# Kernel tuning notes

Hardware: AMD Instinct MI355X
Metric: run time of the kernel (lower is better)

The kernel has to match this reference:

```python
import jax, jax.numpy as jnp
import numpy as np

HIDDEN = 1024
STATE = 16
EXPAND = 2
INNER = HIDDEN * EXPAND
BATCH, SEQ = 4, 2048


def setup_inputs() -> dict:
    key = jax.random.key(0)
    ks = jax.random.split(key, 12)
    s = 0.02
    return {
        "x": jax.random.normal(ks[0], (BATCH, SEQ, HIDDEN), jnp.float32),
        "norm_scale": jnp.ones((HIDDEN,), jnp.float32),
        "norm_bias": jnp.zeros((HIDDEN,), jnp.float32),
        "W_in": jax.random.normal(ks[1], (HIDDEN, 2 * INNER), jnp.float32) * s,
        "conv_w": jax.random.normal(ks[2], (INNER, 3), jnp.float32) * 0.3,
        "conv_b": jnp.zeros((INNER,), jnp.float32),
        "W_dt": jax.random.normal(ks[3], (INNER, INNER), jnp.float32) * s,
        "b_dt": jnp.zeros((INNER,), jnp.float32),
        "A_log": jax.random.normal(ks[4], (INNER, STATE), jnp.float32),
        "D_param": jnp.ones((INNER,), jnp.float32),
        "W_B": jax.random.normal(ks[5], (INNER, STATE), jnp.float32) * s,
        "W_C": jax.random.normal(ks[6], (INNER, STATE), jnp.float32) * s,
        "W_out": jax.random.normal(ks[7], (INNER, HIDDEN), jnp.float32) * s,
    }


def reference(x, norm_scale, norm_bias, W_in, conv_w, conv_b, W_dt, b_dt,
              A_log, D_param, W_B, W_C, W_out):
    residual = x
    # LayerNorm (eps = 1e-5, matches nn.LayerNorm default)
    mu = jnp.mean(x, axis=-1, keepdims=True)
    var = jnp.mean(jnp.square(x - mu), axis=-1, keepdims=True)
    xn = (x - mu) * jax.lax.rsqrt(var + 1e-5) * norm_scale + norm_bias

    xz = xn @ W_in                         # [B, L, 2*inner]
    xb, z = jnp.split(xz, 2, axis=-1)      # each [B, L, inner]

    # depthwise conv1d, kernel 3, padding 1 (cross-correlation as in torch)
    xp = jnp.pad(xb, ((0, 0), (1, 1), (0, 0)))
    xb = (conv_w[:, 0] * xp[:, :-2] + conv_w[:, 1] * xp[:, 1:-1]
          + conv_w[:, 2] * xp[:, 2:] + conv_b)
    xb = jax.nn.silu(xb)

    dt = jax.nn.softplus(xb @ W_dt + b_dt)  # [B, L, inner]
    A = -jnp.exp(A_log)                     # [inner, N]
    Bi = xb @ W_B                           # [B, L, N]
    Ci = xb @ W_C                           # [B, L, N]

    def step(h, inp):
        x_t, dt_t, B_t, C_t = inp           # [B,D], [B,D], [B,N], [B,N]
        A_bar = jnp.exp(dt_t[:, :, None] * A)                 # [B, D, N]
        h = A_bar * h + (dt_t * x_t)[:, :, None] * B_t[:, None, :]
        y_t = jnp.einsum('bdn,bn->bd', h, C_t)
        return h, y_t

    h0 = jnp.zeros((x.shape[0], INNER, STATE), x.dtype)
    xs = (jnp.swapaxes(xb, 0, 1), jnp.swapaxes(dt, 0, 1),
          jnp.swapaxes(Bi, 0, 1), jnp.swapaxes(Ci, 0, 1))
    _, y = jax.lax.scan(step, h0, xs)       # y: [L, B, D]
    y = jnp.swapaxes(y, 0, 1)

    y = (y + D_param * xb) * jax.nn.silu(z)
    return residual + y @ W_out
```

## Files before the change

kernel.cpp:

```cpp
#include <hip/hip_runtime.h>
#include <hip/hip_bf16.h>
#include <cstdint>
#include <cstddef>

#define B_DIM 4
#define L_DIM 2048
#define H_DIM 1024
#define D_DIM 2048
#define N_STATE 16
#define TOKENS (B_DIM * L_DIM)
#define CH 16
#define LC (L_DIM / CH)
#define NEXT 2304
#define NLIM2 2080

typedef __bf16 bf16x8 __attribute__((ext_vector_type(8)));
typedef float f32x4 __attribute__((ext_vector_type(4)));

__device__ __forceinline__ float sigmoidf_(float x) { return 1.f / (1.f + __expf(-x)); }
__device__ __forceinline__ float softplusf_(float x) {
  return fmaxf(x, 0.f) + log1pf(__expf(-fabsf(x)));
}
__device__ __forceinline__ void gl_lds16(const void* g, void* l) {
  __builtin_amdgcn_global_load_lds(
      (const __attribute__((address_space(1))) unsigned int*)g,
      (__attribute__((address_space(3))) unsigned int*)l, 16, 0, 0);
}

__global__ __launch_bounds__(256) void ln_kernel(const float* __restrict__ x,
    const float* __restrict__ gamma, const float* __restrict__ beta,
    __hip_bfloat16* __restrict__ out) {
  int row = blockIdx.x;
  int t = threadIdx.x;
  const float* px = x + (size_t)row * H_DIM;
  float4 v = *(const float4*)(px + t * 4);
  float s  = v.x + v.y + v.z + v.w;
  float ss = v.x * v.x + v.y * v.y + v.z * v.z + v.w * v.w;
  for (int off = 32; off > 0; off >>= 1) {
    s  += __shfl_down(s, off);
    ss += __shfl_down(ss, off);
  }
  __shared__ float red[8];
  __shared__ float stats[2];
  int wave = t >> 6, lane = t & 63;
  if (lane == 0) { red[wave] = s; red[4 + wave] = ss; }
  __syncthreads();
  if (t == 0) {
    float S  = red[0] + red[1] + red[2] + red[3];
    float SS = red[4] + red[5] + red[6] + red[7];
    float mu = S / H_DIM;
    float var = SS / H_DIM - mu * mu;
    stats[0] = mu;
    stats[1] = rsqrtf(var + 1e-5f);
  }
  __syncthreads();
  float mu = stats[0], rstd = stats[1];
  float4 g  = *(const float4*)(gamma + t * 4);
  float4 bt = *(const float4*)(beta + t * 4);
  __hip_bfloat16* po = out + (size_t)row * H_DIM + t * 4;
  po[0] = __float2bfloat16((v.x - mu) * rstd * g.x + bt.x);
  po[1] = __float2bfloat16((v.y - mu) * rstd * g.y + bt.y);
  po[2] = __float2bfloat16((v.z - mu) * rstd * g.z + bt.z);
  po[3] = __float2bfloat16((v.w - mu) * rstd * g.w + bt.w);
}

__global__ void transpose_bf16(const float* __restrict__ in,
                               __hip_bfloat16* __restrict__ out, int R, int C) {
  __shared__ float tile[32][33];
  int c0 = blockIdx.x * 32, r0 = blockIdx.y * 32;
  int tx = threadIdx.x, ty = threadIdx.y;
  for (int i = 0; i < 32; i += 8)
    tile[ty + i][tx] = in[(size_t)(r0 + ty + i) * C + c0 + tx];
  __syncthreads();
  for (int i = 0; i < 32; i += 8)
    out[(size_t)(c0 + ty + i) * R + r0 + tx] = __float2bfloat16(tile[tx][ty + i]);
}

__global__ __launch_bounds__(256) void wbc_transpose(const float* __restrict__ WB,
    const float* __restrict__ WC, __hip_bfloat16* __restrict__ Wext) {
  int tid = blockIdx.x * 256 + threadIdx.x;
  int c = tid & 31;
  int k0 = (tid >> 5) * 16;
  const float* W = (c < 16) ? WB : WC;
  int cc = c & 15;
  __hip_bfloat16* o = Wext + (size_t)(2048 + c) * D_DIM + k0;
  for (int kk = 0; kk < 16; ++kk)
    o[kk] = __float2bfloat16(W[(size_t)(k0 + kk) * N_STATE + cc]);
}

template <int MODE>
__global__ __launch_bounds__(512, 2) void gemm256(
    const __hip_bfloat16* __restrict__ A, const __hip_bfloat16* __restrict__ Bt,
    void* __restrict__ C0, void* __restrict__ C1, int nsplit, int nlimit,
    int K, int lda, int ldb, int ldc, int ntn,
    const float* __restrict__ bias, const float* __restrict__ resid) {
  __shared__ __hip_bfloat16 lds[65536];
  const int t = threadIdx.x;
  const int nwg = gridDim.x;
  int bid = blockIdx.x;
  int wgid = (bid & 7) * (nwg >> 3) + (bid >> 3);
  const int m0 = (wgid / ntn) * 256;
  const int n0 = (wgid % ntn) * 256;

  const int wave = t >> 6, lane = t & 63;
  const int wm = wave >> 2, wn = wave & 3;
  const int l16 = lane & 15, quad = lane >> 4;
  const int bh = wn >> 1;

  const int srow = t >> 3, cslot = t & 7;
  const int cdata = cslot ^ (srow & 7);
  const __hip_bfloat16* Ast = A + (size_t)(m0 + srow) * lda + cdata * 8;
  const __hip_bfloat16* Bst = Bt + (size_t)(n0 + srow) * ldb + cdata * 8;
  const int stoff = srow * 64 + cslot * 8;

  const int ch0 = quad ^ (l16 & 7);
  const int ch1 = ch0 ^ 4;
  const int aoff0 = wm * 8192 + l16 * 64 + ch0 * 8;
  const int aoff1 = wm * 8192 + l16 * 64 + ch1 * 8;
  const int boff0 = 16384 + bh * 8192 + ((wn & 1) * 64 + l16) * 64 + ch0 * 8;
  const int boff1 = 16384 + bh * 8192 + ((wn & 1) * 64 + l16) * 64 + ch1 * 8;

  const int NT = K >> 6;

#define STAGE_HT(dstb, mat, h, ktX) do {                                        \
    const __hip_bfloat16* g_ = ((mat) ? Bst : Ast)                              \
        + (size_t)((h) * 128) * ((mat) ? ldb : lda) + (size_t)(ktX) * 64;       \
    __hip_bfloat16* l_ = &lds[(dstb) + (mat) * 16384 + (h) * 8192 + stoff];     \
    gl_lds16(g_, l_);                                                           \
    gl_lds16(g_ + (size_t)64 * ((mat) ? ldb : lda), l_ + 4096);                 \
  } while (0)

#define RD_A(aP, i0, db_) do {                                                  \
    aP[0][0] = *(const bf16x8*)&lds[(db_) + aoff0 + (i0) * 1024];               \
    aP[0][1] = *(const bf16x8*)&lds[(db_) + aoff1 + (i0) * 1024];               \
    aP[1][0] = *(const bf16x8*)&lds[(db_) + aoff0 + ((i0) + 1) * 1024];         \
    aP[1][1] = *(const bf16x8*)&lds[(db_) + aoff1 + ((i0) + 1) * 1024];         \
  } while (0)

#define RD_B(db_) do {                                                          \
    _Pragma("unroll") for (int j = 0; j < 4; ++j) {                             \
      bB0[j] = *(const bf16x8*)&lds[(db_) + boff0 + j * 1024];                  \
      bB1[j] = *(const bf16x8*)&lds[(db_) + boff1 + j * 1024];                  \
    }                                                                           \
  } while (0)

#define MFMA_PAIR(aP, i0) do {                                                  \
    _Pragma("unroll") for (int j = 0; j < 4; ++j) {                             \
      acc[i0][j] = __builtin_amdgcn_mfma_f32_16x16x32_bf16(                     \
          aP[0][0], bB0[j], acc[i0][j], 0, 0, 0);                               \
      acc[i0][j] = __builtin_amdgcn_mfma_f32_16x16x32_bf16(                     \
          aP[0][1], bB1[j], acc[i0][j], 0, 0, 0);                               \
      acc[(i0) + 1][j] = __builtin_amdgcn_mfma_f32_16x16x32_bf16(               \
          aP[1][0], bB0[j], acc[(i0) + 1][j], 0, 0, 0);                         \
      acc[(i0) + 1][j] = __builtin_amdgcn_mfma_f32_16x16x32_bf16(               \
          aP[1][1], bB1[j], acc[(i0) + 1][j], 0, 0, 0);                         \
    }                                                                           \
  } while (0)

  f32x4 acc[8][4] = {};
  bf16x8 bB0[4], bB1[4];
  bf16x8 a01[2][2], a23[2][2], a45[2][2], a67[2][2];

  STAGE_HT(0, 1, 0, 0);
  STAGE_HT(0, 1, 1, 0);
  STAGE_HT(0, 0, 0, 0);
  STAGE_HT(0, 0, 1, 0);
  STAGE_HT(32768, 1, 0, 1);
  STAGE_HT(32768, 1, 1, 1);
  STAGE_HT(32768, 0, 0, 1);
  asm volatile("s_waitcnt vmcnt(6)" ::: "memory");
  __builtin_amdgcn_s_barrier();

  for (int kt = 0; kt < NT; ++kt) {
    const int db32 = (kt & 1) << 15;
    const int dn32 = db32 ^ 32768;
    const bool p1 = (kt + 1 < NT);
    const bool p2 = (kt + 2 < NT);
    RD_B(db32);
    RD_A(a01, 0, db32);
    if (p1) STAGE_HT(dn32, 0, 1, kt + 1);
    __builtin_amdgcn_s_barrier();
    __builtin_amdgcn_s_setprio(1);
    MFMA_PAIR(a01, 0);
    __builtin_amdgcn_s_setprio(0);
    __builtin_amdgcn_s_barrier();
    RD_A(a23, 2, db32);
    RD_A(a45, 4, db32);
    if (p2) STAGE_HT(db32, 1, 0, kt + 2);
    __builtin_amdgcn_s_barrier();
    __builtin_amdgcn_s_setprio(1);
    MFMA_PAIR(a23, 2);
    __builtin_amdgcn_s_setprio(0);
    __builtin_amdgcn_s_barrier();
    RD_A(a67, 6, db32);
    if (p2) STAGE_HT(db32, 1, 1, kt + 2);
    __builtin_amdgcn_s_barrier();
    __builtin_amdgcn_s_setprio(1);
    MFMA_PAIR(a45, 4);
    __builtin_amdgcn_s_setprio(0);
    __builtin_amdgcn_s_barrier();
    if (p2) STAGE_HT(db32, 0, 0, kt + 2);
    __builtin_amdgcn_s_barrier();
    __builtin_amdgcn_s_setprio(1);
    MFMA_PAIR(a67, 6);
    __builtin_amdgcn_s_setprio(0);
    if (p2) {
      asm volatile("s_waitcnt vmcnt(6)" ::: "memory");
    } else {
      asm volatile("s_waitcnt vmcnt(0)" ::: "memory");
    }
    __builtin_amdgcn_s_barrier();
  }

  const int row_base = m0 + wm * 128;
  const int col_base = n0 + wn * 64;
#pragma unroll
  for (int i = 0; i < 8; ++i) {
    const int row0 = row_base + i * 16 + quad * 4;
#pragma unroll
    for (int j = 0; j < 4; ++j) {
      const int col = col_base + j * 16 + l16;
      f32x4 v = acc[i][j];
      if (MODE == 0) {
#pragma unroll
        for (int r = 0; r < 4; ++r) {
          size_t idx = (size_t)(row0 + r) * ldc + col;
          ((float*)C0)[idx] = v[r] + resid[idx];
        }
      } else if (MODE == 1) {
        bool mainc = (col < nsplit);
        __hip_bfloat16* cb = mainc ? (__hip_bfloat16*)C0 : (__hip_bfloat16*)C1;
        int ccol = mainc ? col : col - nsplit;
#pragma unroll
        for (int r = 0; r < 4; ++r)
          cb[(size_t)(row0 + r) * ldc + ccol] = __float2bfloat16(v[r]);
      } else {
        if (col < nsplit) {
          float bb = bias[col];
#pragma unroll
          for (int r = 0; r < 4; ++r)
            ((__hip_bfloat16*)C0)[(size_t)(row0 + r) * ldc + col] =
                __float2bfloat16(softplusf_(v[r] + bb));
        } else if (col < nlimit) {
#pragma unroll
          for (int r = 0; r < 4; ++r)
            ((float*)C1)[(size_t)(row0 + r) * 128 + (col - nsplit)] = v[r];
        }
      }
    }
  }
#undef STAGE_HT
#undef RD_A
#undef RD_B
#undef MFMA_PAIR
}

#define BM 128
#define BN 128
#define BK 64

template <int MODE>
__global__ __launch_bounds__(256) void gemm_bf16(
    const __hip_bfloat16* __restrict__ A, const __hip_bfloat16* __restrict__ Bt,
    void* __restrict__ C0, void* __restrict__ C1, int nsplit,
    int K, int lda, int ldb, int ldc, int gx,
    const float* __restrict__ bias, const float* __restrict__ resid) {
  __shared__ __hip_bfloat16 As[BM * BK];
  __shared__ __hip_bfloat16 Bs[BN * BK];
  int t = threadIdx.x;
  int bid = blockIdx.x;
  int nsup = gx << 3;
  int super = bid / nsup;
  int rem = bid - super * nsup;
  int m0 = (super * 8 + (rem & 7)) * BM;
  int n0 = (rem >> 3) * BN;

  int wave = t >> 6, lane = t & 63;
  int quad = lane >> 4, l16 = lane & 15;
  int wm = (wave >> 1) * 64, wn = (wave & 1) * 64;

  f32x4 acc[4][4] = {};

  int srow  = t >> 3;
  int cslot = t & 7;
  int cdata = cslot ^ (srow & 7);
  const __hip_bfloat16* Ag[4];
  const __hip_bfloat16* Bg[4];
  __hip_bfloat16* Asl[4];
  __hip_bfloat16* Bsl[4];
#pragma unroll
  for (int j = 0; j < 4; ++j) {
    Ag[j]  = A  + (size_t)(m0 + j * 32 + srow) * lda + cdata * 8;
    Bg[j]  = Bt + (size_t)(n0 + j * 32 + srow) * ldb + cdata * 8;
    Asl[j] = &As[(j * 32 + srow) * BK + cslot * 8];
    Bsl[j] = &Bs[(j * 32 + srow) * BK + cslot * 8];
  }

  for (int k0 = 0; k0 < K; k0 += BK) {
    __syncthreads();
#pragma unroll
    for (int j = 0; j < 4; ++j) {
      gl_lds16(Ag[j] + k0, Asl[j]);
      gl_lds16(Bg[j] + k0, Bsl[j]);
    }
    __syncthreads();
#pragma unroll
    for (int s = 0; s < 2; ++s) {
      int cs = ((s * 4 + quad) ^ (l16 & 7)) * 8;
      bf16x8 af[4], bf_[4];
#pragma unroll
      for (int i = 0; i < 4; ++i) {
        af[i]  = *(const bf16x8*)&As[(wm + i * 16 + l16) * BK + cs];
        bf_[i] = *(const bf16x8*)&Bs[(wn + i * 16 + l16) * BK + cs];
      }
#pragma unroll
      for (int i = 0; i < 4; ++i)
#pragma unroll
        for (int j = 0; j < 4; ++j)
          acc[i][j] = __builtin_amdgcn_mfma_f32_16x16x32_bf16(af[i], bf_[j], acc[i][j], 0, 0, 0);
    }
  }

#pragma unroll
  for (int i = 0; i < 4; ++i) {
    int row0 = m0 + wm + i * 16 + quad * 4;
#pragma unroll
    for (int j = 0; j < 4; ++j) {
      int col = n0 + wn + j * 16 + l16;
      f32x4 v = acc[i][j];
      if (MODE == 0) {
#pragma unroll
        for (int r = 0; r < 4; ++r) {
          size_t idx = (size_t)(row0 + r) * ldc + col;
          ((float*)C0)[idx] = v[r] + resid[idx];
        }
      } else if (MODE == 1) {
        bool mainc = (col < nsplit);
        __hip_bfloat16* cb = mainc ? (__hip_bfloat16*)C0 : (__hip_bfloat16*)C1;
        int ccol = mainc ? col : col - nsplit;
#pragma unroll
        for (int r = 0; r < 4; ++r)
          cb[(size_t)(row0 + r) * ldc + ccol] = __float2bfloat16(v[r]);
      } else {
        if (col < nsplit) {
          float bb = bias[col];
#pragma unroll
          for (int r = 0; r < 4; ++r)
            ((__hip_bfloat16*)C0)[(size_t)(row0 + r) * ldc + col] =
                __float2bfloat16(softplusf_(v[r] + bb));
        } else {
#pragma unroll
          for (int r = 0; r < 4; ++r)
            ((float*)C1)[(size_t)(row0 + r) * 128 + (col - nsplit)] = v[r];
        }
      }
    }
  }
}

__global__ __launch_bounds__(256) void conv_silu_kernel(const __hip_bfloat16* __restrict__ xb,
    const float* __restrict__ cw, const float* __restrict__ cb,
    __hip_bfloat16* __restrict__ xbc) {
  size_t i2 = (size_t)blockIdx.x * 256 + threadIdx.x;
  int dp = (int)(i2 & (D_DIM / 2 - 1));
  size_t tok = i2 >> 10;
  int l = (int)(tok & (L_DIM - 1));
  int d = dp * 2;
  const __hip_bfloat162* base = (const __hip_bfloat162*)xb + i2;
  __hip_bfloat162 cc = base[0];
  float v0 = cw[d * 3 + 1] * __bfloat162float(cc.x) + cb[d];
  float v1 = cw[d * 3 + 4] * __bfloat162float(cc.y) + cb[d + 1];
  if (l > 0) {
    __hip_bfloat162 pm = base[-(D_DIM / 2)];
    v0 += cw[d * 3 + 0] * __bfloat162float(pm.x);
    v1 += cw[d * 3 + 3] * __bfloat162float(pm.y);
  }
  if (l < L_DIM - 1) {
    __hip_bfloat162 pp = base[D_DIM / 2];
    v0 += cw[d * 3 + 2] * __bfloat162float(pp.x);
    v1 += cw[d * 3 + 5] * __bfloat162float(pp.y);
  }
  v0 = v0 * sigmoidf_(v0);
  v1 = v1 * sigmoidf_(v1);
  __hip_bfloat162 o;
  o.x = __float2bfloat16(v0);
  o.y = __float2bfloat16(v1);
  ((__hip_bfloat162*)xbc)[i2] = o;
}

__global__ __launch_bounds__(256) void scan1_kernel(const __hip_bfloat16* __restrict__ dt,
    const __hip_bfloat16* __restrict__ xbc, const float* __restrict__ BiCi,
    const float* __restrict__ A_log, float* __restrict__ hfin,
    float* __restrict__ dtsum) {
  __shared__ float Bsh[LC * N_STATE];
  int t = threadIdx.x;
  int d = blockIdx.x * 256 + t;
  int c = blockIdx.y, b = blockIdx.z;
  size_t base = (size_t)b * L_DIM + (size_t)c * LC;
  for (int idx = t; idx < LC * 4; idx += 256) {
    int row = idx >> 2, q = idx & 3;
    ((float4*)Bsh)[row * 4 + q] = *(const float4*)&BiCi[(base + row) * 128 + q * 4];
  }
  float Aneg[N_STATE];
  {
    const float4* Ap = (const float4*)(A_log + (size_t)d * N_STATE);
#pragma unroll
    for (int q = 0; q < 4; ++q) {
      float4 av = Ap[q];
      Aneg[4 * q + 0] = -__expf(av.x);
      Aneg[4 * q + 1] = -__expf(av.y);
      Aneg[4 * q + 2] = -__expf(av.z);
      Aneg[4 * q + 3] = -__expf(av.w);
    }
  }
  __syncthreads();
  const __hip_bfloat16* dtp = dt + base * D_DIM + d;
  const __hip_bfloat16* xp = xbc + base * D_DIM + d;
  float h[N_STATE];
#pragma unroll
  for (int n = 0; n < N_STATE; ++n) h[n] = 0.f;
  float ds = 0.f;
  float dtv = __bfloat162float(dtp[0]), xv = __bfloat162float(xp[0]);
  for (int i = 0; i < LC; ++i) {
    int ip = (i < LC - 1) ? i + 1 : i;
    float dt2 = __bfloat162float(dtp[(size_t)ip * D_DIM]);
    float x2  = __bfloat162float(xp[(size_t)ip * D_DIM]);
    float dtx = dtv * xv;
    ds += dtv;
    const float4* Brow = (const float4*)&Bsh[i * N_STATE];
#pragma unroll
    for (int q = 0; q < 4; ++q) {
      float4 bv = Brow[q];
      h[4*q+0] = __expf(dtv * Aneg[4*q+0]) * h[4*q+0] + dtx * bv.x;
      h[4*q+1] = __expf(dtv * Aneg[4*q+1]) * h[4*q+1] + dtx * bv.y;
      h[4*q+2] = __expf(dtv * Aneg[4*q+2]) * h[4*q+2] + dtx * bv.z;
      h[4*q+3] = __expf(dtv * Aneg[4*q+3]) * h[4*q+3] + dtx * bv.w;
    }
    dtv = dt2; xv = x2;
  }
  float* ho = hfin + (((size_t)b * CH + c) * D_DIM + d) * N_STATE;
#pragma unroll
  for (int q = 0; q < 4; ++q) {
    float4 v; v.x = h[4*q]; v.y = h[4*q+1]; v.z = h[4*q+2]; v.w = h[4*q+3];
    ((float4*)ho)[q] = v;
  }
  dtsum[((size_t)b * CH + c) * D_DIM + d] = ds;
}

__global__ __launch_bounds__(256) void scan2_kernel(const float* __restrict__ hfin,
    const float* __restrict__ dtsum, const float* __restrict__ A_log,
    float* __restrict__ hstart) {
  int tid = blockIdx.x * 256 + threadIdx.x;
  int n = tid & 15;
  int d = (tid >> 4) & (D_DIM - 1);
  int b = tid >> 15;
  float Aneg = -__expf(A_log[d * N_STATE + n]);
  float run = 0.f;
  for (int c = 0; c < CH; ++c) {
    size_t o = (((size_t)b * CH + c) * D_DIM + d) * N_STATE + n;
    hstart[o] = run;
    run = __expf(Aneg * dtsum[((size_t)b * CH + c) * D_DIM + d]) * run + hfin[o];
  }
}

__global__ __launch_bounds__(256) void scan3_kernel(const __hip_bfloat16* __restrict__ dt,
    const __hip_bfloat16* __restrict__ xbc, const float* __restrict__ BiCi,
    const float* __restrict__ A_log,
    const float* __restrict__ hstart, const __hip_bfloat16* __restrict__ z,
    const float* __restrict__ Dp, __hip_bfloat16* __restrict__ yo) {
  __shared__ float Bsh[LC * N_STATE];
  __shared__ float Csh[LC * N_STATE];
  int t = threadIdx.x;
  int d = blockIdx.x * 256 + t;
  int c = blockIdx.y, b = blockIdx.z;
  size_t base = (size_t)b * L_DIM + (size_t)c * LC;
  for (int idx = t; idx < LC * 4; idx += 256) {
    int row = idx >> 2, q = idx & 3;
    ((float4*)Bsh)[row * 4 + q] = *(const float4*)&BiCi[(base + row) * 128 + q * 4];
    ((float4*)Csh)[row * 4 + q] = *(const float4*)&BiCi[(base + row) * 128 + 16 + q * 4];
  }
  float Aneg[N_STATE];
  {
    const float4* Ap = (const float4*)(A_log + (size_t)d * N_STATE);
#pragma unroll
    for (int q = 0; q < 4; ++q) {
      float4 av = Ap[q];
      Aneg[4 * q + 0] = -__expf(av.x);
      Aneg[4 * q + 1] = -__expf(av.y);
      Aneg[4 * q + 2] = -__expf(av.z);
      Aneg[4 * q + 3] = -__expf(av.w);
    }
  }
  float h[N_STATE];
  {
    const float4* hs = (const float4*)(hstart + (((size_t)b * CH + c) * D_DIM + d) * N_STATE);
#pragma unroll
    for (int q = 0; q < 4; ++q) {
      float4 v = hs[q];
      h[4*q] = v.x; h[4*q+1] = v.y; h[4*q+2] = v.z; h[4*q+3] = v.w;
    }
  }
  float Dv = Dp[d];
  __syncthreads();
  const __hip_bfloat16* dtp = dt + base * D_DIM + d;
  const __hip_bfloat16* xp = xbc + base * D_DIM + d;
  const __hip_bfloat16* zp = z + base * D_DIM + d;
  __hip_bfloat16* yp = yo + base * D_DIM + d;
  float dtv = __bfloat162float(dtp[0]), xv = __bfloat162float(xp[0]);
  float zv = __bfloat162float(zp[0]);
  for (int i = 0; i < LC; ++i) {
    int ip = (i < LC - 1) ? i + 1 : i;
    float dt2 = __bfloat162float(dtp[(size_t)ip * D_DIM]);
    float x2  = __bfloat162float(xp[(size_t)ip * D_DIM]);
    float z2  = __bfloat162float(zp[(size_t)ip * D_DIM]);
    float dtx = dtv * xv;
    const float4* Brow = (const float4*)&Bsh[i * N_STATE];
    const float4* Crow = (const float4*)&Csh[i * N_STATE];
    float yv = 0.f;
#pragma unroll
    for (int q = 0; q < 4; ++q) {
      float4 bv = Brow[q];
      float4 cv = Crow[q];
      h[4*q+0] = __expf(dtv * Aneg[4*q+0]) * h[4*q+0] + dtx * bv.x;
      h[4*q+1] = __expf(dtv * Aneg[4*q+1]) * h[4*q+1] + dtx * bv.y;
      h[4*q+2] = __expf(dtv * Aneg[4*q+2]) * h[4*q+2] + dtx * bv.z;
      h[4*q+3] = __expf(dtv * Aneg[4*q+3]) * h[4*q+3] + dtx * bv.w;
      yv += h[4*q+0] * cv.x + h[4*q+1] * cv.y + h[4*q+2] * cv.z + h[4*q+3] * cv.w;
    }
    float g = zv * sigmoidf_(zv);
    yp[(size_t)i * D_DIM] = __float2bfloat16((yv + Dv * xv) * g);
    dtv = dt2; xv = x2; zv = z2;
  }
}

extern "C" void kernel_launch(void* const* d_in, const int* in_sizes, int n_in,
                              void* d_out, int out_size, void* d_ws, size_t ws_size,
                              hipStream_t stream) {
  const float* x          = (const float*)d_in[0];
  const float* norm_scale = (const float*)d_in[1];
  const float* norm_bias  = (const float*)d_in[2];
  const float* W_in       = (const float*)d_in[3];
  const float* conv_w     = (const float*)d_in[4];
  const float* conv_b     = (const float*)d_in[5];
  const float* W_dt       = (const float*)d_in[6];
  const float* b_dt       = (const float*)d_in[7];
  const float* A_log      = (const float*)d_in[8];
  const float* D_param    = (const float*)d_in[9];
  const float* W_B        = (const float*)d_in[10];
  const float* W_C        = (const float*)d_in[11];
  const float* W_out      = (const float*)d_in[12];
  float* out = (float*)d_out;

  const size_t MB = 1024 * 1024;
  const size_t NEEDED = 193 * MB;
  if (ws_size < NEEDED) return;

  char* ws = (char*)d_ws;
  __hip_bfloat16* xn     = (__hip_bfloat16*)(ws);
  __hip_bfloat16* W_outT = (__hip_bfloat16*)(ws);
  float*          hfin   = (float*)(ws + 4 * MB);
  float*          dtsum  = (float*)(ws + 12 * MB);
  __hip_bfloat16* xb     = (__hip_bfloat16*)(ws + 16 * MB);
  __hip_bfloat16* ybf    = (__hip_bfloat16*)(ws + 16 * MB);
  __hip_bfloat16* z      = (__hip_bfloat16*)(ws + 48 * MB);
  __hip_bfloat16* xbc    = (__hip_bfloat16*)(ws + 80 * MB);
  __hip_bfloat16* dtY    = (__hip_bfloat16*)(ws + 112 * MB);
  float*          BiCi   = (float*)(ws + 144 * MB);
  __hip_bfloat16* W_ext  = (__hip_bfloat16*)(ws + 148 * MB);
  __hip_bfloat16* W_inT  = (__hip_bfloat16*)(ws + 177 * MB);
  float*          hstart = (float*)(ws + 177 * MB);

  dim3 tb(32, 8);
  transpose_bf16<<<dim3(4096 / 32, 1024 / 32), tb, 0, stream>>>(W_in, W_inT, 1024, 4096);
  transpose_bf16<<<dim3(2048 / 32, 2048 / 32), tb, 0, stream>>>(W_dt, W_ext, 2048, 2048);
  wbc_transpose<<<16, 256, 0, stream>>>(W_B, W_C, W_ext);
  ln_kernel<<<TOKENS, 256, 0, stream>>>(x, norm_scale, norm_bias, xn);
  gemm256<1><<<(TOKENS / 256) * (4096 / 256), 512, 0, stream>>>(
      xn, W_inT, xb, z, D_DIM, 1 << 30, H_DIM, H_DIM, H_DIM, D_DIM, 4096 / 256,
      nullptr, nullptr);
  transpose_bf16<<<dim3(1024 / 32, 2048 / 32), tb, 0, stream>>>(W_out, W_outT, 2048, 1024);
  conv_silu_kernel<<<(TOKENS * D_DIM / 2) / 256, 256, 0, stream>>>(xb, conv_w, conv_b, xbc);
  gemm256<2><<<(TOKENS / 256) * (NEXT / 256), 512, 0, stream>>>(
      xbc, W_ext, dtY, BiCi, D_DIM, NLIM2, D_DIM, D_DIM, D_DIM, D_DIM, NEXT / 256,
      b_dt, nullptr);
  scan1_kernel<<<dim3(D_DIM / 256, CH, B_DIM), 256, 0, stream>>>(
      dtY, xbc, BiCi, A_log, hfin, dtsum);
  scan2_kernel<<<(B_DIM * D_DIM * N_STATE) / 256, 256, 0, stream>>>(
      hfin, dtsum, A_log, hstart);
  scan3_kernel<<<dim3(D_DIM / 256, CH, B_DIM), 256, 0, stream>>>(
      dtY, xbc, BiCi, A_log, hstart, z, D_param, ybf);
  gemm_bf16<0><<<(H_DIM / BN) * (TOKENS / BM), 256, 0, stream>>>(
      ybf, W_outT, out, nullptr, 1 << 30, D_DIM, D_DIM, D_DIM, H_DIM, H_DIM / BN,
      nullptr, x);
}
```

Before: 646.9 us.

## Double-buffer gemm_bf16, relax gemm256 occupancy, and double scan chunk count

The change doubles the scan chunk count so the chunked scan has more parallel work, and relocates the workspace buffers to fit the larger per-chunk state. It drops gemm256's launch bound to one block per SM and adds an explicit LDS-count wait before each MFMA phase. It also double-buffers the 128x128 GEMM so global-to-LDS loads for the next K tile overlap with MFMAs on the current one, cutting one barrier per iteration. These trade extra LDS use and a longer serial second scan pass for more overlap and parallelism, and the buffer moves risk overlapping workspace regions.

```diff
diff --git a/kernel.cpp b/kernel.cpp
--- a/kernel.cpp
+++ b/kernel.cpp
@@ -9,7 +9,7 @@
 #define D_DIM 2048
 #define N_STATE 16
 #define TOKENS (B_DIM * L_DIM)
-#define CH 16
+#define CH 32
 #define LC (L_DIM / CH)
 #define NEXT 2304
 #define NLIM2 2080
@@ -89,7 +89,7 @@
 }
 
 template <int MODE>
-__global__ __launch_bounds__(512, 2) void gemm256(
+__global__ __launch_bounds__(512, 1) void gemm256(
     const __hip_bfloat16* __restrict__ A, const __hip_bfloat16* __restrict__ Bt,
     void* __restrict__ C0, void* __restrict__ C1, int nsplit, int nlimit,
     int K, int lda, int ldb, int ldc, int ntn,
@@ -157,6 +157,17 @@
     }                                                                           \
   } while (0)
 
+#define PH_GATE() do {                                                          \
+    __builtin_amdgcn_s_barrier();                                               \
+    asm volatile("s_waitcnt lgkmcnt(0)" ::: "memory");                          \
+    __builtin_amdgcn_s_setprio(1);                                              \
+  } while (0)
+
+#define PH_END() do {                                                           \
+    __builtin_amdgcn_s_setprio(0);                                              \
+    __builtin_amdgcn_s_barrier();                                               \
+  } while (0)
+
   f32x4 acc[8][4] = {};
   bf16x8 bB0[4], bB1[4];
   bf16x8 a01[2][2], a23[2][2], a45[2][2], a67[2][2];
@@ -179,26 +190,20 @@
     RD_B(db32);
     RD_A(a01, 0, db32);
     if (p1) STAGE_HT(dn32, 0, 1, kt + 1);
-    __builtin_amdgcn_s_barrier();
-    __builtin_amdgcn_s_setprio(1);
+    PH_GATE();
     MFMA_PAIR(a01, 0);
-    __builtin_amdgcn_s_setprio(0);
-    __builtin_amdgcn_s_barrier();
+    PH_END();
     RD_A(a23, 2, db32);
     RD_A(a45, 4, db32);
     if (p2) STAGE_HT(db32, 1, 0, kt + 2);
-    __builtin_amdgcn_s_barrier();
-    __builtin_amdgcn_s_setprio(1);
+    PH_GATE();
     MFMA_PAIR(a23, 2);
-    __builtin_amdgcn_s_setprio(0);
-    __builtin_amdgcn_s_barrier();
+    PH_END();
     RD_A(a67, 6, db32);
     if (p2) STAGE_HT(db32, 1, 1, kt + 2);
-    __builtin_amdgcn_s_barrier();
-    __builtin_amdgcn_s_setprio(1);
+    PH_GATE();
     MFMA_PAIR(a45, 4);
-    __builtin_amdgcn_s_setprio(0);
-    __builtin_amdgcn_s_barrier();
+    PH_END();
     if (p2) STAGE_HT(db32, 0, 0, kt + 2);
     __builtin_amdgcn_s_barrier();
     __builtin_amdgcn_s_setprio(1);
@@ -253,6 +258,8 @@
 #undef RD_A
 #undef RD_B
 #undef MFMA_PAIR
+#undef PH_GATE
+#undef PH_END
 }
 
 #define BM 128
@@ -265,8 +272,8 @@
     void* __restrict__ C0, void* __restrict__ C1, int nsplit,
     int K, int lda, int ldb, int ldc, int gx,
     const float* __restrict__ bias, const float* __restrict__ resid) {
-  __shared__ __hip_bfloat16 As[BM * BK];
-  __shared__ __hip_bfloat16 Bs[BN * BK];
+  __shared__ __hip_bfloat16 As[2 * BM * BK];
+  __shared__ __hip_bfloat16 Bs[2 * BN * BK];
   int t = threadIdx.x;
   int bid = blockIdx.x;
   int nsup = gx << 3;
@@ -286,32 +293,42 @@
   int cdata = cslot ^ (srow & 7);
   const __hip_bfloat16* Ag[4];
   const __hip_bfloat16* Bg[4];
-  __hip_bfloat16* Asl[4];
-  __hip_bfloat16* Bsl[4];
+  int soff[4];
 #pragma unroll
   for (int j = 0; j < 4; ++j) {
     Ag[j]  = A  + (size_t)(m0 + j * 32 + srow) * lda + cdata * 8;
     Bg[j]  = Bt + (size_t)(n0 + j * 32 + srow) * ldb + cdata * 8;
-    Asl[j] = &As[(j * 32 + srow) * BK + cslot * 8];
-    Bsl[j] = &Bs[(j * 32 + srow) * BK + cslot * 8];
-  }
-
-  for (int k0 = 0; k0 < K; k0 += BK) {
-    __syncthreads();
-#pragma unroll
-    for (int j = 0; j < 4; ++j) {
-      gl_lds16(Ag[j] + k0, Asl[j]);
-      gl_lds16(Bg[j] + k0, Bsl[j]);
-    }
-    __syncthreads();
+    soff[j] = (j * 32 + srow) * BK + cslot * 8;
+  }
+
+  const int NT = K / BK;
+#pragma unroll
+  for (int j = 0; j < 4; ++j) {
+    gl_lds16(Ag[j], &As[soff[j]]);
+    gl_lds16(Bg[j], &Bs[soff[j]]);
+  }
+  asm volatile("s_waitcnt vmcnt(0)" ::: "memory");
+  __builtin_amdgcn_s_barrier();
+
+  for (int kt = 0; kt < NT; ++kt) {
+    const int cur = (kt & 1) * (BM * BK);
+    const int nxt = cur ^ (BM * BK);
+    if (kt + 1 < NT) {
+      const int k1 = (kt + 1) * BK;
+#pragma unroll
+      for (int j = 0; j < 4; ++j) {
+        gl_lds16(Ag[j] + k1, &As[nxt + soff[j]]);
+        gl_lds16(Bg[j] + k1, &Bs[nxt + soff[j]]);
+      }
+    }
 #pragma unroll
     for (int s = 0; s < 2; ++s) {
       int cs = ((s * 4 + quad) ^ (l16 & 7)) * 8;
       bf16x8 af[4], bf_[4];
 #pragma unroll
       for (int i = 0; i < 4; ++i) {
-        af[i]  = *(const bf16x8*)&As[(wm + i * 16 + l16) * BK + cs];
-        bf_[i] = *(const bf16x8*)&Bs[(wn + i * 16 + l16) * BK + cs];
+        af[i]  = *(const bf16x8*)&As[cur + (wm + i * 16 + l16) * BK + cs];
+        bf_[i] = *(const bf16x8*)&Bs[cur + (wn + i * 16 + l16) * BK + cs];
       }
 #pragma unroll
       for (int i = 0; i < 4; ++i)
@@ -319,6 +336,8 @@
         for (int j = 0; j < 4; ++j)
           acc[i][j] = __builtin_amdgcn_mfma_f32_16x16x32_bf16(af[i], bf_[j], acc[i][j], 0, 0, 0);
     }
+    asm volatile("s_waitcnt vmcnt(0)" ::: "memory");
+    __builtin_amdgcn_s_barrier();
   }
 
 #pragma unroll
@@ -558,8 +577,6 @@
   char* ws = (char*)d_ws;
   __hip_bfloat16* xn     = (__hip_bfloat16*)(ws);
   __hip_bfloat16* W_outT = (__hip_bfloat16*)(ws);
-  float*          hfin   = (float*)(ws + 4 * MB);
-  float*          dtsum  = (float*)(ws + 12 * MB);
   __hip_bfloat16* xb     = (__hip_bfloat16*)(ws + 16 * MB);
   __hip_bfloat16* ybf    = (__hip_bfloat16*)(ws + 16 * MB);
   __hip_bfloat16* z      = (__hip_bfloat16*)(ws + 48 * MB);
@@ -567,8 +584,10 @@
   __hip_bfloat16* dtY    = (__hip_bfloat16*)(ws + 112 * MB);
   float*          BiCi   = (float*)(ws + 144 * MB);
   __hip_bfloat16* W_ext  = (__hip_bfloat16*)(ws + 148 * MB);
+  float*          hstart = (float*)(ws + 158 * MB);
+  float*          dtsum  = (float*)(ws + 174 * MB);
   __hip_bfloat16* W_inT  = (__hip_bfloat16*)(ws + 177 * MB);
-  float*          hstart = (float*)(ws + 177 * MB);
+  float*          hfin   = (float*)(ws + 177 * MB);
 
   dim3 tb(32, 8);
   transpose_bf16<<<dim3(4096 / 32, 1024 / 32), tb, 0, stream>>>(W_in, W_inT, 1024, 4096);
```

After: 639.4 us. No clear change (-1.2%).
